# Kernel optimization log

Hardware: AMD Instinct MI355X
Metric: run time of the kernel (lower is better)

## Reference

```python
import jax, jax.numpy as jnp
import numpy as np

EMBEDDING_DIM = 64
NUM_EMBEDDINGS = 1024
BETA = 0.25


def setup_inputs() -> dict:
    key = jax.random.key(0)
    k1, k2 = jax.random.split(key)
    inputs = jax.random.normal(k1, (64, 32, 32, EMBEDDING_DIM), dtype=jnp.float32)
    rand_range = 1.0 / NUM_EMBEDDINGS
    embeddings = jax.random.uniform(
        k2, (EMBEDDING_DIM, NUM_EMBEDDINGS),
        minval=-rand_range, maxval=rand_range, dtype=jnp.float32)
    return {"inputs": inputs, "embeddings": embeddings}


def reference(inputs, embeddings):
    # Flatten to [N, D]
    flat = inputs.reshape(-1, EMBEDDING_DIM)
    distances = (jnp.sum(flat ** 2, axis=1, keepdims=True)
                 - 2.0 * (flat @ embeddings)
                 + jnp.sum(embeddings ** 2, axis=0, keepdims=True))  # [N, K]
    encoding_indices = jnp.argmax(-distances, axis=1)
    encoding_indices = encoding_indices.reshape(inputs.shape[:-1])
    # Embedding lookup: codebook is [D, K], gather columns
    quantized = embeddings.T[encoding_indices]  # [..., D]
    e_latent_loss = jnp.mean((jax.lax.stop_gradient(quantized) - inputs) ** 2)
    q_latent_loss = jnp.mean((quantized - jax.lax.stop_gradient(inputs)) ** 2)
    loss = e_latent_loss + q_latent_loss * BETA
    # Straight-through estimator
    quantized = inputs + jax.lax.stop_gradient(quantized - inputs)
    return (quantized, loss, encoding_indices)
```

## Files before the change

kernel.cpp:

```cpp
#include <hip/hip_runtime.h>
#include <math.h>

#define EMB_D 64
#define EMB_K 1024
#define NROWS 65536
#define QELEMS (NROWS * EMB_D)


__global__ __launch_bounds__(256) void prep_kernel(const float* __restrict__ E,
                                                   float* __restrict__ Et,
                                                   float* __restrict__ esq,
                                                   double* lsum) {
    int k = blockIdx.x * 256 + threadIdx.x;
    if (k == 0) *lsum = 0.0;
    if (k >= EMB_K) return;
    float s = 0.f;
#pragma unroll
    for (int d = 0; d < EMB_D; ++d) {
        float v = E[d * EMB_K + k];
        Et[k * EMB_D + d] = v;
        s = fmaf(v, v, s);
    }
    esq[k] = s;
}

#define DOT4(acc, q, e)                                    \
    do {                                                   \
        acc = fmaf((q).x, (e).x, acc);                     \
        acc = fmaf((q).y, (e).y, acc);                     \
        acc = fmaf((q).z, (e).z, acc);                     \
        acc = fmaf((q).w, (e).w, acc);                     \
    } while (0)

__global__ __launch_bounds__(256, 4) void main_kernel(const float* __restrict__ X,
                                                      const float* __restrict__ Et,
                                                      const float* __restrict__ esq,
                                                      float* __restrict__ quant,
                                                      float* __restrict__ idxf,
                                                      double* lsum) {
    __shared__ float sd[4][64];
    __shared__ int   si[4][64];
    __shared__ int   sidx[64];

    const int lane = threadIdx.x & 63;
    const int w    = threadIdx.x >> 6;
    const int rowbase = blockIdx.x * 64;

    const float4* xr = reinterpret_cast<const float4*>(X + (size_t)(rowbase + lane) * EMB_D);
    float4 x0 = xr[0],  x1 = xr[1],  x2 = xr[2],  x3 = xr[3];
    float4 x4 = xr[4],  x5 = xr[5],  x6 = xr[6],  x7 = xr[7];
    float4 x8 = xr[8],  x9 = xr[9],  x10 = xr[10], x11 = xr[11];
    float4 x12 = xr[12], x13 = xr[13], x14 = xr[14], x15 = xr[15];

    float xsq = 0.f;
    DOT4(xsq, x0, x0);   DOT4(xsq, x1, x1);   DOT4(xsq, x2, x2);   DOT4(xsq, x3, x3);
    DOT4(xsq, x4, x4);   DOT4(xsq, x5, x5);   DOT4(xsq, x6, x6);   DOT4(xsq, x7, x7);
    DOT4(xsq, x8, x8);   DOT4(xsq, x9, x9);   DOT4(xsq, x10, x10); DOT4(xsq, x11, x11);
    DOT4(xsq, x12, x12); DOT4(xsq, x13, x13); DOT4(xsq, x14, x14); DOT4(xsq, x15, x15);

    asm volatile("" ::: "memory");

    const int k0 = __builtin_amdgcn_readfirstlane(w) * (EMB_K / 4);

    float bestd = INFINITY;
    int   besti = 0;
    for (int k = k0; k < k0 + EMB_K / 4; k += 2) {
        const float4* e0 = reinterpret_cast<const float4*>(Et + (size_t)k * EMB_D);
        const float4* e1 = e0 + 16;
        float d0 = 0.f, d1 = 0.f;
#define STEP(i) { float4 a = e0[i]; float4 b = e1[i]; DOT4(d0, x##i, a); DOT4(d1, x##i, b); }
        STEP(0)  STEP(1)  STEP(2)  STEP(3)
        STEP(4)  STEP(5)  STEP(6)  STEP(7)
        STEP(8)  STEP(9)  STEP(10) STEP(11)
        STEP(12) STEP(13) STEP(14) STEP(15)
#undef STEP
        float dist0 = (xsq - 2.0f * d0) + esq[k];
        float dist1 = (xsq - 2.0f * d1) + esq[k + 1];
        if (dist0 < bestd) { bestd = dist0; besti = k; }
        if (dist1 < bestd) { bestd = dist1; besti = k + 1; }
    }
    sd[w][lane] = bestd;
    si[w][lane] = besti;
    __syncthreads();

    if (threadIdx.x < 64) {
        float bd = sd[0][lane];
        int   bi = si[0][lane];
#pragma unroll
        for (int u = 1; u < 4; ++u) {
            if (sd[u][lane] < bd) { bd = sd[u][lane]; bi = si[u][lane]; }
        }
        sidx[lane] = bi;
        idxf[rowbase + lane] = (float)bi;
    }
    __syncthreads();

    {
        const int r = threadIdx.x >> 2;
        const int p = threadIdx.x & 3;
        const int k = sidx[r];
        const float4* xq = reinterpret_cast<const float4*>(X + (size_t)(rowbase + r) * EMB_D) + p * 4;
        const float4* qq = reinterpret_cast<const float4*>(Et + (size_t)k * EMB_D) + p * 4;
        float4*       oq = reinterpret_cast<float4*>(quant + (size_t)(rowbase + r) * EMB_D) + p * 4;
        float ps = 0.f;
#pragma unroll
        for (int u = 0; u < 4; ++u) {
            float4 xx = xq[u];
            float4 q  = qq[u];
            float dx = q.x - xx.x, dy = q.y - xx.y, dz = q.z - xx.z, dw = q.w - xx.w;
            oq[u] = make_float4(xx.x + dx, xx.y + dy, xx.z + dz, xx.w + dw);
            ps += dx * dx + dy * dy + dz * dz + dw * dw;
        }
#pragma unroll
        for (int off = 32; off > 0; off >>= 1) ps += __shfl_down(ps, off, 64);
        if (lane == 0) atomicAdd(lsum, (double)ps);
    }
}

__global__ void finalize_kernel(const double* lsum, float* loss_out) {
    double m = *lsum / (double)QELEMS;
    *loss_out = (float)(m + 0.25 * m);
}

extern "C" void kernel_launch(void* const* d_in, const int* in_sizes, int n_in,
                              void* d_out, int out_size, void* d_ws, size_t ws_size,
                              hipStream_t stream) {
    const float* X = (const float*)d_in[0];
    const float* E = (const float*)d_in[1];

    float* out = (float*)d_out;
    float* quant = out;
    float* loss  = out + QELEMS;
    float* idxf  = out + QELEMS + 1;

    char* ws = (char*)d_ws;
    float*  Et   = (float*)(ws);
    float*  esq  = (float*)(ws + 262144);
    double* lsum = (double*)(ws + 266240);

    prep_kernel<<<4, 256, 0, stream>>>(E, Et, esq, lsum);
    main_kernel<<<NROWS / 64, 256, 0, stream>>>(X, Et, esq, quant, idxf, lsum);
    finalize_kernel<<<1, 1, 0, stream>>>(lsum, loss);
}
```

Before: 240.4 us.

## Swizzle codebook into 8-code blocks and stage input rows in LDS

The codebook is transposed into interleaved blocks of 8 codes, so each inner step loads 8 codes' float4 slices that sit next to each other in memory. Each thread now keeps 8 dot-product accumulators instead of 2. Input rows are staged through padded shared memory with coalesced loads instead of per-thread register copies, and the final write-back pass reuses them. This trades register-resident x for LDS reads in the hot loop, which lowers register pressure, but it adds LDS traffic and drops the occupancy hint from the launch bounds.

```diff
diff --git a/kernel.cpp b/kernel.cpp
--- a/kernel.cpp
+++ b/kernel.cpp
@@ -7,23 +7,6 @@
 #define QELEMS (NROWS * EMB_D)
 
 
-__global__ __launch_bounds__(256) void prep_kernel(const float* __restrict__ E,
-                                                   float* __restrict__ Et,
-                                                   float* __restrict__ esq,
-                                                   double* lsum) {
-    int k = blockIdx.x * 256 + threadIdx.x;
-    if (k == 0) *lsum = 0.0;
-    if (k >= EMB_K) return;
-    float s = 0.f;
-#pragma unroll
-    for (int d = 0; d < EMB_D; ++d) {
-        float v = E[d * EMB_K + k];
-        Et[k * EMB_D + d] = v;
-        s = fmaf(v, v, s);
-    }
-    esq[k] = s;
-}
-
 #define DOT4(acc, q, e)                                    \
     do {                                                   \
         acc = fmaf((q).x, (e).x, acc);                     \
@@ -32,58 +15,103 @@
         acc = fmaf((q).w, (e).w, acc);                     \
     } while (0)
 
-__global__ __launch_bounds__(256, 4) void main_kernel(const float* __restrict__ X,
-                                                      const float* __restrict__ Et,
-                                                      const float* __restrict__ esq,
-                                                      float* __restrict__ quant,
-                                                      float* __restrict__ idxf,
-                                                      double* lsum) {
+__global__ __launch_bounds__(256) void prep_kernel(const float* __restrict__ E,
+                                                   float* __restrict__ Etsw,
+                                                   float* __restrict__ esq,
+                                                   double* lsum) {
+    const int k = blockIdx.x * 256 + threadIdx.x;
+    if (k == 0) *lsum = 0.0;
+    float s = 0.f;
+    float* dst = Etsw + (size_t)(k >> 3) * 512 + (k & 7) * 4;
+#pragma unroll
+    for (int j = 0; j < 16; ++j) {
+        float4 q;
+        q.x = E[(j * 4 + 0) * EMB_K + k];
+        q.y = E[(j * 4 + 1) * EMB_K + k];
+        q.z = E[(j * 4 + 2) * EMB_K + k];
+        q.w = E[(j * 4 + 3) * EMB_K + k];
+        s = fmaf(q.x, q.x, s); s = fmaf(q.y, q.y, s);
+        s = fmaf(q.z, q.z, s); s = fmaf(q.w, q.w, s);
+        *reinterpret_cast<float4*>(dst + j * 32) = q;
+    }
+    esq[k] = s;
+}
+
+__global__ __launch_bounds__(256) void main_kernel(const float* X,
+                                                   const float* __restrict__ Etsw,
+                                                   const float* __restrict__ esq,
+                                                   float* __restrict__ quant,
+                                                   float* __restrict__ idxf,
+                                                   double* lsum) {
+    __shared__ __align__(16) float xs[64 * 68];
     __shared__ float sd[4][64];
     __shared__ int   si[4][64];
     __shared__ int   sidx[64];
 
-    const int lane = threadIdx.x & 63;
-    const int w    = threadIdx.x >> 6;
+    const int tid  = threadIdx.x;
+    const int lane = tid & 63;
+    const int w    = tid >> 6;
     const int rowbase = blockIdx.x * 64;
 
-    const float4* xr = reinterpret_cast<const float4*>(X + (size_t)(rowbase + lane) * EMB_D);
-    float4 x0 = xr[0],  x1 = xr[1],  x2 = xr[2],  x3 = xr[3];
-    float4 x4 = xr[4],  x5 = xr[5],  x6 = xr[6],  x7 = xr[7];
-    float4 x8 = xr[8],  x9 = xr[9],  x10 = xr[10], x11 = xr[11];
-    float4 x12 = xr[12], x13 = xr[13], x14 = xr[14], x15 = xr[15];
+#pragma unroll
+    for (int u = 0; u < 4; ++u) {
+        int m = u * 256 + tid;
+        int r = m >> 4, j = m & 15;
+        float4 v = reinterpret_cast<const float4*>(X)[(size_t)(rowbase + r) * 16 + j];
+        *reinterpret_cast<float4*>(&xs[r * 68 + j * 4]) = v;
+    }
+    __syncthreads();
+
+    const float* xrow = &xs[lane * 68];
 
     float xsq = 0.f;
-    DOT4(xsq, x0, x0);   DOT4(xsq, x1, x1);   DOT4(xsq, x2, x2);   DOT4(xsq, x3, x3);
-    DOT4(xsq, x4, x4);   DOT4(xsq, x5, x5);   DOT4(xsq, x6, x6);   DOT4(xsq, x7, x7);
-    DOT4(xsq, x8, x8);   DOT4(xsq, x9, x9);   DOT4(xsq, x10, x10); DOT4(xsq, x11, x11);
-    DOT4(xsq, x12, x12); DOT4(xsq, x13, x13); DOT4(xsq, x14, x14); DOT4(xsq, x15, x15);
-
-    asm volatile("" ::: "memory");
+#pragma unroll
+    for (int j = 0; j < 16; ++j) {
+        float4 x4 = *reinterpret_cast<const float4*>(xrow + j * 4);
+        DOT4(xsq, x4, x4);
+    }
 
     const int k0 = __builtin_amdgcn_readfirstlane(w) * (EMB_K / 4);
 
     float bestd = INFINITY;
     int   besti = 0;
-    for (int k = k0; k < k0 + EMB_K / 4; k += 2) {
-        const float4* e0 = reinterpret_cast<const float4*>(Et + (size_t)k * EMB_D);
-        const float4* e1 = e0 + 16;
-        float d0 = 0.f, d1 = 0.f;
-#define STEP(i) { float4 a = e0[i]; float4 b = e1[i]; DOT4(d0, x##i, a); DOT4(d1, x##i, b); }
-        STEP(0)  STEP(1)  STEP(2)  STEP(3)
-        STEP(4)  STEP(5)  STEP(6)  STEP(7)
-        STEP(8)  STEP(9)  STEP(10) STEP(11)
-        STEP(12) STEP(13) STEP(14) STEP(15)
-#undef STEP
-        float dist0 = (xsq - 2.0f * d0) + esq[k];
-        float dist1 = (xsq - 2.0f * d1) + esq[k + 1];
-        if (dist0 < bestd) { bestd = dist0; besti = k; }
-        if (dist1 < bestd) { bestd = dist1; besti = k + 1; }
+    for (int b = 0; b < 32; ++b) {
+        const int kb = k0 + b * 8;
+        const float* eb = Etsw + (size_t)(kb >> 3) * 512;
+        float a0 = 0.f, a1 = 0.f, a2 = 0.f, a3 = 0.f;
+        float a4 = 0.f, a5 = 0.f, a6 = 0.f, a7 = 0.f;
+#pragma unroll
+        for (int j = 0; j < 16; ++j) {
+            const float4 x4 = *reinterpret_cast<const float4*>(xrow + j * 4);
+            const float4* ej = reinterpret_cast<const float4*>(eb + j * 32);
+            float4 e0 = ej[0], e1 = ej[1], e2 = ej[2], e3 = ej[3];
+            float4 e4 = ej[4], e5 = ej[5], e6 = ej[6], e7 = ej[7];
+            DOT4(a0, x4, e0); DOT4(a1, x4, e1); DOT4(a2, x4, e2); DOT4(a3, x4, e3);
+            DOT4(a4, x4, e4); DOT4(a5, x4, e5); DOT4(a6, x4, e6); DOT4(a7, x4, e7);
+        }
+        const float* eq = esq + kb;
+        float q0 = (xsq - 2.0f * a0) + eq[0];
+        float q1 = (xsq - 2.0f * a1) + eq[1];
+        float q2 = (xsq - 2.0f * a2) + eq[2];
+        float q3 = (xsq - 2.0f * a3) + eq[3];
+        float q4 = (xsq - 2.0f * a4) + eq[4];
+        float q5 = (xsq - 2.0f * a5) + eq[5];
+        float q6 = (xsq - 2.0f * a6) + eq[6];
+        float q7 = (xsq - 2.0f * a7) + eq[7];
+        if (q0 < bestd) { bestd = q0; besti = kb + 0; }
+        if (q1 < bestd) { bestd = q1; besti = kb + 1; }
+        if (q2 < bestd) { bestd = q2; besti = kb + 2; }
+        if (q3 < bestd) { bestd = q3; besti = kb + 3; }
+        if (q4 < bestd) { bestd = q4; besti = kb + 4; }
+        if (q5 < bestd) { bestd = q5; besti = kb + 5; }
+        if (q6 < bestd) { bestd = q6; besti = kb + 6; }
+        if (q7 < bestd) { bestd = q7; besti = kb + 7; }
     }
     sd[w][lane] = bestd;
     si[w][lane] = besti;
     __syncthreads();
 
-    if (threadIdx.x < 64) {
+    if (tid < 64) {
         float bd = sd[0][lane];
         int   bi = si[0][lane];
 #pragma unroll
@@ -96,17 +124,18 @@
     __syncthreads();
 
     {
-        const int r = threadIdx.x >> 2;
-        const int p = threadIdx.x & 3;
+        const int r = tid >> 2;
+        const int p = tid & 3;
         const int k = sidx[r];
-        const float4* xq = reinterpret_cast<const float4*>(X + (size_t)(rowbase + r) * EMB_D) + p * 4;
-        const float4* qq = reinterpret_cast<const float4*>(Et + (size_t)k * EMB_D) + p * 4;
-        float4*       oq = reinterpret_cast<float4*>(quant + (size_t)(rowbase + r) * EMB_D) + p * 4;
+        const float* xrp = &xs[r * 68 + p * 16];
+        const float* qb  = Etsw + (size_t)(k >> 3) * 512 + (k & 7) * 4;
+        float4* oq = reinterpret_cast<float4*>(quant + (size_t)(rowbase + r) * EMB_D) + p * 4;
         float ps = 0.f;
 #pragma unroll
         for (int u = 0; u < 4; ++u) {
-            float4 xx = xq[u];
-            float4 q  = qq[u];
+            int j = p * 4 + u;
+            float4 xx = *reinterpret_cast<const float4*>(xrp + u * 4);
+            float4 q  = *reinterpret_cast<const float4*>(qb + j * 32);
             float dx = q.x - xx.x, dy = q.y - xx.y, dz = q.z - xx.z, dw = q.w - xx.w;
             oq[u] = make_float4(xx.x + dx, xx.y + dy, xx.z + dz, xx.w + dw);
             ps += dx * dx + dy * dy + dz * dz + dw * dw;
@@ -134,11 +163,11 @@
     float* idxf  = out + QELEMS + 1;
 
     char* ws = (char*)d_ws;
-    float*  Et   = (float*)(ws);
+    float*  Etsw = (float*)(ws);
     float*  esq  = (float*)(ws + 262144);
     double* lsum = (double*)(ws + 266240);
 
-    prep_kernel<<<4, 256, 0, stream>>>(E, Et, esq, lsum);
-    main_kernel<<<NROWS / 64, 256, 0, stream>>>(X, Et, esq, quant, idxf, lsum);
+    prep_kernel<<<EMB_K / 256, 256, 0, stream>>>(E, Etsw, esq, lsum);
+    main_kernel<<<NROWS / 64, 256, 0, stream>>>(X, Etsw, esq, quant, idxf, lsum);
     finalize_kernel<<<1, 1, 0, stream>>>(lsum, loss);
 }
```

After: 247.9 us. 1.03x slower.
